# Performance work log

Measured on AMD Instinct MI355X. Metric: run time of the kernel, lower is better.

The kernel has to match this reference:

```python
import jax, jax.numpy as jnp
import numpy as np

B, N = 16, 512


def _line_coords(n):
    # Discrete Fourier slice coordinates for all mValues (center=False, ridgelet=False).
    mu = n + n // 2 if n % 2 == 0 else n + 1
    p = 2 if n % 2 == 0 else n
    m = jnp.arange(mu)           # [mu]
    k = jnp.arange(n)            # [N]
    lt = (m < n)[:, None]        # m < N branch mask, [mu, 1]
    # m < N:  row = k,                 col = (k*m) % N
    # m >= N: row = (k*p*(m-N)) % N,   col = k
    row = jnp.where(lt, k[None, :], (k[None, :] * p * (m[:, None] - n)) % n)
    col = jnp.where(lt, (k[None, :] * m[:, None]) % n, k[None, :])
    return row, col  # each [mu, N] int32


def setup_inputs() -> dict:
    key = jax.random.key(0)
    return {"image": jax.random.normal(key, (B, N, N), dtype=jnp.float32)}


def reference(image):
    b, n, _ = image.shape
    row, col = _line_coords(n)                                   # [mu, N]
    dft = jnp.fft.fft2(image.astype(jnp.complex64), norm="ortho")  # [B, N, N] c64
    slices = dft[:, row, col]                                    # gather -> [B, mu, N]
    sino = jnp.fft.ifft(slices, norm="ortho")                    # [B, mu, N] c64
    # complex sinogram returned as stacked (real, imag) float channels
    return jnp.stack([sino.real, sino.imag], axis=-1)            # [B, mu, N, 2]
```

## Files before the change

### kernel.cpp

```cpp
#include <hip/hip_runtime.h>


#define NN 512
#define MU 768
#define MASK 511
#define SCALE 0.04419417382415922f

__global__ __launch_bounds__(512) void k_init(const float* __restrict__ img,
                                              float* __restrict__ A0) {
  __shared__ float T[4][64][33];
  const int bx = blockIdx.x, b = blockIdx.y;
  const int xp = bx >> 3, wt = bx & 7;
  const int x0 = xp * 64, x1 = x0 + 256, w0 = wt * 32;
  const float* src = img + (size_t)b * NN * NN;
  float* dst = A0 + (size_t)b * (512 * NN);

  for (int idx = threadIdx.x; idx < 2048; idx += 512) {
    const int tile = idx >> 9;
    const int r = (idx >> 3) & 63, c4 = (idx & 7) << 2;
    const int xb = (tile & 2) ? x1 : x0;
    const int wb = (tile & 1) ? (w0 + 256) : w0;
    const float4 v = *(const float4*)&src[(size_t)(xb + r) * NN + wb + c4];
    T[tile][r][c4]     = v.x;
    T[tile][r][c4 + 1] = v.y;
    T[tile][r][c4 + 2] = v.z;
    T[tile][r][c4 + 3] = v.w;
  }
  __syncthreads();
  for (int idx = threadIdx.x; idx < 2048; idx += 512) {
    const int s = idx >> 9;
    const int wl = (idx >> 4) & 31, x4 = (idx & 15) << 2;
    const int ta = (s & 2) ? 2 : 0;
    const int tb = (s == 0) ? 1 : (s == 1) ? 3 : (s == 2) ? 3 : 1;
    const int rbase = ((s & 1) ? 256 : 0) + w0;
    const int cbase = (s & 2) ? x1 : x0;
    float4 a;
    a.x = T[ta][x4][wl]     + T[tb][x4][wl];
    a.y = T[ta][x4 + 1][wl] + T[tb][x4 + 1][wl];
    a.z = T[ta][x4 + 2][wl] + T[tb][x4 + 2][wl];
    a.w = T[ta][x4 + 3][wl] + T[tb][x4 + 3][wl];
    *(float4*)&dst[(size_t)(rbase + wl) * NN + cbase + x4] = a;
  }
}

__global__ __launch_bounds__(512) void k_pass1(const float* __restrict__ A0,
                                               const float* __restrict__ img,
                                               float* __restrict__ A1,
                                               float* __restrict__ B1) {
  __shared__ float L[16 * 512];
  const int bx = blockIdx.x, b = blockIdx.y;
  const int t = threadIdx.x;
  const bool isB = bx >= 32;
  const int c = isB ? 0 : (bx >> 4);
  const int w = isB ? (bx - 32) : (bx & 15);
  if (isB) {
    const float4* s4 = (const float4*)(img + (size_t)b * NN * NN);
    float4* l4 = (float4*)L;
    for (int it = 0; it < 4; ++it) {
      int flat = it * 512 + t;
      int lrow = flat >> 7, col = flat & 127;
      float4 u = s4[(w + 16 * lrow) * 128 + col];
      float4 v = s4[(w + 16 * lrow + 256) * 128 + col];
      u.x += v.x; u.y += v.y; u.z += v.z; u.w += v.w;
      l4[lrow * 128 + col] = u;
    }
  } else {
    const float4* s4 = (const float4*)(A0 + (size_t)b * 512 * NN);
    float4* l4 = (float4*)L;
    const int pbase = c * 256 + w;
    for (int it = 0; it < 4; ++it) {
      int flat = it * 512 + t;
      int lrow = flat >> 7, col = flat & 127;
      l4[lrow * 128 + col] = s4[(pbase + 16 * lrow) * 128 + col];
    }
  }
  __syncthreads();
  const int g = t >> 7;
  const int x4 = (t & 127) * 4;
  const int C0 = isB ? (2 * g) : (c + 2 * g);
  float* outA = A1 + (size_t)b * 512 * NN;
  float* outB = B1 + (size_t)b * 256 * NN;
  float4 acc[4];
#pragma unroll
  for (int jj = 0; jj < 4; ++jj) acc[jj] = make_float4(0.f, 0.f, 0.f, 0.f);
#pragma unroll
  for (int bb = 0; bb < 16; ++bb) {
    const int p = ((bb & 3) == 0) ? 1 : (((bb & 1) == 0) ? 2 : 4);
    const int step = (128 * bb) & MASK;
    int base = (x4 - C0 * bb * 16) & MASK;
    float4 v[4];
#pragma unroll
    for (int k = 0; k < 4; ++k)
      if (k < p) {
        v[k] = *(const float4*)&L[bb * 512 + base];
        base = (base - step) & MASK;
      }
#pragma unroll
    for (int jj = 0; jj < 4; ++jj) {
      const float4 u = v[jj & (p - 1)];
      acc[jj].x += u.x; acc[jj].y += u.y; acc[jj].z += u.z; acc[jj].w += u.w;
    }
  }
#pragma unroll
  for (int jj = 0; jj < 4; ++jj) {
    const int j = 4 * jj + g;
    const int C = C0 + 8 * jj;
    const int orow = isB ? (j * 16 + w) : (C * 16 + w);
    float* op = isB ? outB : outA;
    *(float4*)&op[(size_t)orow * NN + x4] = acc[jj];
  }
}

__global__ __launch_bounds__(512) void k_pass2(const float* __restrict__ A1,
                                               const float* __restrict__ B1,
                                               float2* __restrict__ out) {
  __shared__ float L[16 * 512];
  const int bx = blockIdx.x, b = blockIdx.y;
  const int t = threadIdx.x;
  const bool isB = bx >= 32;
  const int c = isB ? 2 * (bx - 32) : bx;
  const float* in = isB ? (B1 + (size_t)b * 256 * NN + (size_t)(c >> 1) * 16 * NN)
                        : (A1 + (size_t)b * 512 * NN + (size_t)c * 16 * NN);
  {
    const float4* s4 = (const float4*)in;
    float4* l4 = (float4*)L;
    for (int it = 0; it < 4; ++it) l4[it * 512 + t] = s4[it * 512 + t];
  }
  __syncthreads();
  float acc[16];
#pragma unroll
  for (int j = 0; j < 16; ++j) acc[j] = 0.f;
#pragma unroll
  for (int bb = 0; bb < 16; ++bb) {
    const int p = (bb == 0) ? 1
                : ((bb & 1) ? 16 : ((bb & 2) ? 8 : ((bb & 4) ? 4 : 2)));
    const int step = (32 * bb) & MASK;
    const float* row = L + bb * 512;
    int base = (t - c * bb) & MASK;
    float v[16];
#pragma unroll
    for (int k = 0; k < 16; ++k)
      if (k < p) {
        v[k] = row[base];
        base = (base - step) & MASK;
      }
#pragma unroll
    for (int j = 0; j < 16; ++j) acc[j] += v[j & (p - 1)];
  }
#pragma unroll
  for (int j = 0; j < 16; ++j) {
    int m = isB ? (512 + (c >> 1) + 16 * j) : (c + 32 * j);
    float2 o; o.x = acc[j] * SCALE; o.y = 0.f;
    out[((size_t)b * MU + m) * NN + t] = o;
  }
}

#define TM 16
#define YT 16
#define LDS_STRIDE 516
__global__ __launch_bounds__(512) void drt_main(const float* __restrict__ img,
                                                float* __restrict__ out) {
  __shared__ float rows[YT * LDS_STRIDE];
  const int b = blockIdx.y;
  const int tile = blockIdx.x;
  const int t = threadIdx.x;
  const bool caseB = (tile >= 32);
  const int a0 = caseB ? (tile - 32) * TM : tile * TM;
  const float* __restrict__ src = img + (size_t)b * (NN * NN);
  const int slope0 = caseB ? (2 * a0) : a0;
  const int dslope = caseB ? 2 : 1;
  float acc[TM];
#pragma unroll
  for (int i = 0; i < TM; ++i) acc[i] = 0.0f;
  for (int y0 = 0; y0 < NN; y0 += YT) {
    __syncthreads();
    if (caseB) {
#pragma unroll
      for (int r = 0; r < YT; ++r) rows[r * LDS_STRIDE + t] = src[(y0 + r) * NN + t];
    } else {
#pragma unroll
      for (int rep = 0; rep < YT; ++rep) {
        int idx = rep * NN + t;
        int xx = idx >> 4, cc = idx & 15;
        rows[cc * LDS_STRIDE + xx] = src[xx * NN + y0 + cc];
      }
    }
    __syncthreads();
#pragma unroll 4
    for (int r = 0; r < YT; ++r) {
      const int v = y0 + r;
      int base = t - slope0 * v;
      const int step = dslope * v;
      const float* __restrict__ rowp = rows + r * LDS_STRIDE;
#pragma unroll
      for (int i = 0; i < TM; ++i) { acc[i] += rowp[base & MASK]; base -= step; }
    }
  }
  const int m = caseB ? (NN + a0) : a0;
  float2* outp = (float2*)out;
#pragma unroll
  for (int i = 0; i < TM; ++i) {
    float2 vv; vv.x = acc[i] * SCALE; vv.y = 0.0f;
    outp[((size_t)b * MU + (m + i)) * NN + t] = vv;
  }
}

extern "C" void kernel_launch(void* const* d_in, const int* in_sizes, int n_in,
                              void* d_out, int out_size, void* d_ws, size_t ws_size,
                              hipStream_t stream) {
  const float* img = (const float*)d_in[0];
  if (ws_size < (size_t)42 * 1024 * 1024) {
    drt_main<<<dim3(48, 16), dim3(512), 0, stream>>>(img, (float*)d_out);
    return;
  }
  float* W  = (float*)d_ws;
  float* A0 = W;
  float* A1 = W + 4194304;
  float* B1 = W + 8388608;

  k_init <<<dim3(32, 16), dim3(512), 0, stream>>>(img, A0);
  k_pass1<<<dim3(48, 16), dim3(512), 0, stream>>>(A0, img, A1, B1);
  k_pass2<<<dim3(48, 16), dim3(512), 0, stream>>>(A1, B1, (float2*)d_out);
}
```

Before: 98.05 us.

## Move B-branch pass1 into init kernel and use nontemporal output stores

The B-branch blocks of pass1 depend only on the input image, so they are moved into the init kernel and run alongside the A0 transpose-add blocks. Pass1 then only handles the A branch, with 32 blocks instead of 48. This balances the work across the first two launches and shortens the dependent chain. The final complex output writes become nontemporal stores to reduce cache pollution; the cost is a shared-memory footprint sized for the larger of the two branches in the merged kernel.

```diff
diff --git a/kernel.cpp b/kernel.cpp
--- a/kernel.cpp
+++ b/kernel.cpp
@@ -6,65 +6,105 @@
 #define MASK 511
 #define SCALE 0.04419417382415922f
 
-__global__ __launch_bounds__(512) void k_init(const float* __restrict__ img,
-                                              float* __restrict__ A0) {
-  __shared__ float T[4][64][33];
+typedef float f32x2 __attribute__((ext_vector_type(2)));
+
+__global__ __launch_bounds__(512) void k_init_p1b(const float* __restrict__ img,
+                                                  float* __restrict__ A0,
+                                                  float* __restrict__ B1) {
+  __shared__ float S[4 * 64 * 33];
   const int bx = blockIdx.x, b = blockIdx.y;
-  const int xp = bx >> 3, wt = bx & 7;
-  const int x0 = xp * 64, x1 = x0 + 256, w0 = wt * 32;
+  const int t = threadIdx.x;
   const float* src = img + (size_t)b * NN * NN;
-  float* dst = A0 + (size_t)b * (512 * NN);
-
-  for (int idx = threadIdx.x; idx < 2048; idx += 512) {
-    const int tile = idx >> 9;
-    const int r = (idx >> 3) & 63, c4 = (idx & 7) << 2;
-    const int xb = (tile & 2) ? x1 : x0;
-    const int wb = (tile & 1) ? (w0 + 256) : w0;
-    const float4 v = *(const float4*)&src[(size_t)(xb + r) * NN + wb + c4];
-    T[tile][r][c4]     = v.x;
-    T[tile][r][c4 + 1] = v.y;
-    T[tile][r][c4 + 2] = v.z;
-    T[tile][r][c4 + 3] = v.w;
-  }
-  __syncthreads();
-  for (int idx = threadIdx.x; idx < 2048; idx += 512) {
-    const int s = idx >> 9;
-    const int wl = (idx >> 4) & 31, x4 = (idx & 15) << 2;
-    const int ta = (s & 2) ? 2 : 0;
-    const int tb = (s == 0) ? 1 : (s == 1) ? 3 : (s == 2) ? 3 : 1;
-    const int rbase = ((s & 1) ? 256 : 0) + w0;
-    const int cbase = (s & 2) ? x1 : x0;
-    float4 a;
-    a.x = T[ta][x4][wl]     + T[tb][x4][wl];
-    a.y = T[ta][x4 + 1][wl] + T[tb][x4 + 1][wl];
-    a.z = T[ta][x4 + 2][wl] + T[tb][x4 + 2][wl];
-    a.w = T[ta][x4 + 3][wl] + T[tb][x4 + 3][wl];
-    *(float4*)&dst[(size_t)(rbase + wl) * NN + cbase + x4] = a;
-  }
-}
-
-__global__ __launch_bounds__(512) void k_pass1(const float* __restrict__ A0,
-                                               const float* __restrict__ img,
-                                               float* __restrict__ A1,
-                                               float* __restrict__ B1) {
+
+  if (bx < 32) {
+    float (*T)[64][33] = (float (*)[64][33])S;
+    const int xp = bx >> 3, wt = bx & 7;
+    const int x0 = xp * 64, x1 = x0 + 256, w0 = wt * 32;
+    float* dst = A0 + (size_t)b * (512 * NN);
+
+    for (int idx = t; idx < 2048; idx += 512) {
+      const int tile = idx >> 9;
+      const int r = (idx >> 3) & 63, c4 = (idx & 7) << 2;
+      const int xb = (tile & 2) ? x1 : x0;
+      const int wb = (tile & 1) ? (w0 + 256) : w0;
+      const float4 v = *(const float4*)&src[(size_t)(xb + r) * NN + wb + c4];
+      T[tile][r][c4]     = v.x;
+      T[tile][r][c4 + 1] = v.y;
+      T[tile][r][c4 + 2] = v.z;
+      T[tile][r][c4 + 3] = v.w;
+    }
+    __syncthreads();
+    for (int idx = t; idx < 2048; idx += 512) {
+      const int s = idx >> 9;
+      const int wl = (idx >> 4) & 31, x4 = (idx & 15) << 2;
+      const int ta = (s & 2) ? 2 : 0;
+      const int tb = (s == 0) ? 1 : (s == 1) ? 3 : (s == 2) ? 3 : 1;
+      const int rbase = ((s & 1) ? 256 : 0) + w0;
+      const int cbase = (s & 2) ? x1 : x0;
+      float4 a;
+      a.x = T[ta][x4][wl]     + T[tb][x4][wl];
+      a.y = T[ta][x4 + 1][wl] + T[tb][x4 + 1][wl];
+      a.z = T[ta][x4 + 2][wl] + T[tb][x4 + 2][wl];
+      a.w = T[ta][x4 + 3][wl] + T[tb][x4 + 3][wl];
+      *(float4*)&dst[(size_t)(rbase + wl) * NN + cbase + x4] = a;
+    }
+  } else {
+    float* L = S;
+    const int w = bx - 32;
+    {
+      const float4* s4 = (const float4*)src;
+      float4* l4 = (float4*)L;
+      for (int it = 0; it < 4; ++it) {
+        int flat = it * 512 + t;
+        int lrow = flat >> 7, col = flat & 127;
+        float4 u = s4[(w + 16 * lrow) * 128 + col];
+        float4 v = s4[(w + 16 * lrow + 256) * 128 + col];
+        u.x += v.x; u.y += v.y; u.z += v.z; u.w += v.w;
+        l4[lrow * 128 + col] = u;
+      }
+    }
+    __syncthreads();
+    const int g = t >> 7;
+    const int x4 = (t & 127) * 4;
+    const int C0 = 2 * g;
+    float* outB = B1 + (size_t)b * 256 * NN;
+    float4 acc[4];
+#pragma unroll
+    for (int jj = 0; jj < 4; ++jj) acc[jj] = make_float4(0.f, 0.f, 0.f, 0.f);
+#pragma unroll
+    for (int bb = 0; bb < 16; ++bb) {
+      const int p = ((bb & 3) == 0) ? 1 : (((bb & 1) == 0) ? 2 : 4);
+      const int step = (128 * bb) & MASK;
+      int base = (x4 - C0 * bb * 16) & MASK;
+      float4 v[4];
+#pragma unroll
+      for (int k = 0; k < 4; ++k)
+        if (k < p) {
+          v[k] = *(const float4*)&L[bb * 512 + base];
+          base = (base - step) & MASK;
+        }
+#pragma unroll
+      for (int jj = 0; jj < 4; ++jj) {
+        const float4 u = v[jj & (p - 1)];
+        acc[jj].x += u.x; acc[jj].y += u.y; acc[jj].z += u.z; acc[jj].w += u.w;
+      }
+    }
+#pragma unroll
+    for (int jj = 0; jj < 4; ++jj) {
+      const int j = 4 * jj + g;
+      *(float4*)&outB[(size_t)(j * 16 + w) * NN + x4] = acc[jj];
+    }
+  }
+}
+
+__global__ __launch_bounds__(512) void k_pass1A(const float* __restrict__ A0,
+                                                float* __restrict__ A1) {
   __shared__ float L[16 * 512];
   const int bx = blockIdx.x, b = blockIdx.y;
   const int t = threadIdx.x;
-  const bool isB = bx >= 32;
-  const int c = isB ? 0 : (bx >> 4);
-  const int w = isB ? (bx - 32) : (bx & 15);
-  if (isB) {
-    const float4* s4 = (const float4*)(img + (size_t)b * NN * NN);
-    float4* l4 = (float4*)L;
-    for (int it = 0; it < 4; ++it) {
-      int flat = it * 512 + t;
-      int lrow = flat >> 7, col = flat & 127;
-      float4 u = s4[(w + 16 * lrow) * 128 + col];
-      float4 v = s4[(w + 16 * lrow + 256) * 128 + col];
-      u.x += v.x; u.y += v.y; u.z += v.z; u.w += v.w;
-      l4[lrow * 128 + col] = u;
-    }
-  } else {
+  const int c = bx >> 4;
+  const int w = bx & 15;
+  {
     const float4* s4 = (const float4*)(A0 + (size_t)b * 512 * NN);
     float4* l4 = (float4*)L;
     const int pbase = c * 256 + w;
@@ -77,9 +117,8 @@
   __syncthreads();
   const int g = t >> 7;
   const int x4 = (t & 127) * 4;
-  const int C0 = isB ? (2 * g) : (c + 2 * g);
+  const int C0 = c + 2 * g;
   float* outA = A1 + (size_t)b * 512 * NN;
-  float* outB = B1 + (size_t)b * 256 * NN;
   float4 acc[4];
 #pragma unroll
   for (int jj = 0; jj < 4; ++jj) acc[jj] = make_float4(0.f, 0.f, 0.f, 0.f);
@@ -103,11 +142,8 @@
   }
 #pragma unroll
   for (int jj = 0; jj < 4; ++jj) {
-    const int j = 4 * jj + g;
     const int C = C0 + 8 * jj;
-    const int orow = isB ? (j * 16 + w) : (C * 16 + w);
-    float* op = isB ? outB : outA;
-    *(float4*)&op[(size_t)orow * NN + x4] = acc[jj];
+    *(float4*)&outA[(size_t)(C * 16 + w) * NN + x4] = acc[jj];
   }
 }
 
@@ -150,8 +186,8 @@
 #pragma unroll
   for (int j = 0; j < 16; ++j) {
     int m = isB ? (512 + (c >> 1) + 16 * j) : (c + 32 * j);
-    float2 o; o.x = acc[j] * SCALE; o.y = 0.f;
-    out[((size_t)b * MU + m) * NN + t] = o;
+    f32x2 o; o.x = acc[j] * SCALE; o.y = 0.f;
+    __builtin_nontemporal_store(o, (f32x2*)&out[((size_t)b * MU + m) * NN + t]);
   }
 }
 
@@ -218,7 +254,7 @@
   float* A1 = W + 4194304;
   float* B1 = W + 8388608;
 
-  k_init <<<dim3(32, 16), dim3(512), 0, stream>>>(img, A0);
-  k_pass1<<<dim3(48, 16), dim3(512), 0, stream>>>(A0, img, A1, B1);
-  k_pass2<<<dim3(48, 16), dim3(512), 0, stream>>>(A1, B1, (float2*)d_out);
-}
+  k_init_p1b<<<dim3(48, 16), dim3(512), 0, stream>>>(img, A0, B1);
+  k_pass1A  <<<dim3(32, 16), dim3(512), 0, stream>>>(A0, A1);
+  k_pass2   <<<dim3(48, 16), dim3(512), 0, stream>>>(A1, B1, (float2*)d_out);
+}
```

Result: no change. 96.60 us (-1.5%).
